# Kernel tuning notes

Hardware: AMD Instinct MI355X
Metric: run time of the kernel (lower is better)

The kernel has to match this reference:

```python
import jax, jax.numpy as jnp
import numpy as np

T, B, D, H, L = 256, 32, 512, 512, 3  # seq_len, batch, input_size, hidden_size, num_layers


def setup_inputs() -> dict:
    key = jax.random.key(0)
    ks = jax.random.split(key, 18)
    s = 0.02  # small init to keep gates out of saturation
    rn = lambda k, shape: (jax.random.normal(k, shape, dtype=jnp.float32) * s)
    return {
        "x": jax.random.normal(ks[0], (T, B, D), dtype=jnp.float32),
        "h0": jax.random.normal(ks[1], (L, B, H), dtype=jnp.float32),
        "c0": jax.random.normal(ks[2], (L, B, H), dtype=jnp.float32),
        # per-layer gate projections (torch Linear -> W in [in, out] layout)
        "W_i2h": rn(ks[3], (L, D, 3 * H)), "b_i2h": rn(ks[4], (L, 3 * H)),
        "W_h2h": rn(ks[5], (L, H, 3 * H)), "b_h2h": rn(ks[6], (L, 3 * H)),
        "W_wc": rn(ks[7], (L, D, H)),      "b_wc": rn(ks[8], (L, H)),
        # L x L gated-feedback weights: wg(input), ug(concat of all hiddens), uc(per-layer hidden)
        "W_wg": rn(ks[9], (L, L, D, H)),       "b_wg": rn(ks[10], (L, L, H)),
        "W_ug": rn(ks[11], (L, L, L * H, H)),  "b_ug": rn(ks[12], (L, L, H)),
        "W_uc": rn(ks[13], (L, L, H, H)),      "b_uc": rn(ks[14], (L, L, H)),
    }


def reference(x, h0, c0, W_i2h, b_i2h, W_h2h, b_h2h, W_wc, b_wc,
              W_wg, b_wg, W_ug, b_ug, W_uc, b_uc):
    num_layers, Hh = h0.shape[0], h0.shape[2]

    def step(carry, x_t):
        h, c = carry  # [L, B, H] each
        # concat of all previous hidden states along features: [B, L*H]
        nowH = jnp.transpose(h, (1, 0, 2)).reshape(h.shape[1], -1)
        inp = x_t
        hs, cs = [], []
        for l in range(num_layers):
            gates = jax.nn.sigmoid(inp @ W_i2h[l] + b_i2h[l]
                                   + h[l] @ W_h2h[l] + b_h2h[l])  # [B, 3H]
            i_g, f_g, o_g = jnp.split(gates, 3, axis=1)
            # global gates over all source layers _l: [L, B, H]
            gg = jax.nn.sigmoid(
                jnp.einsum('bd,ldh->lbh', inp, W_wg[l]) + b_wg[l][:, None, :]
                + jnp.einsum('bk,lkh->lbh', nowH, W_ug[l]) + b_ug[l][:, None, :])
            # gated contributions from each layer's previous hidden state
            uc = jnp.einsum('lbh,lhk->lbk', h, W_uc[l]) + b_uc[l][:, None, :]
            cand = jnp.tanh(inp @ W_wc[l] + b_wc[l] + jnp.sum(gg * uc, axis=0))
            c_new = f_g * c[l] + i_g * cand
            h_new = o_g * jnp.tanh(c_new)
            hs.append(h_new)
            cs.append(c_new)
            inp = h_new  # dropout == 0 -> identity
        return (jnp.stack(hs), jnp.stack(cs)), hs[-1]

    (h_n, c_n), out = jax.lax.scan(step, (h0, c0), x)
    return out, (h_n, c_n)
```

## Files before the change

kernel.cpp:

```cpp
#include <hip/hip_runtime.h>
#include <math.h>

#define TT 256
#define BB 32
#define DD 512
#define HH 512
#define H3 1536

static constexpr size_t SZ_I2HT = 3ull * H3 * HH;
static constexpr size_t SZ_H2HT = 3ull * H3 * HH;
static constexpr size_t SZ_WCT  = 3ull * HH * HH;
static constexpr size_t SZ_WGT  = 9ull * HH * HH;
static constexpr size_t SZ_UGT  = 9ull * HH * H3;
static constexpr size_t SZ_UCT  = 9ull * HH * HH;
static constexpr size_t SZ_ST   = 3ull * BB * HH;
static constexpr size_t SZ_GH   = 3ull * BB * H3;
static constexpr size_t SZ_UGP  = 3ull * 9 * BB * HH;
static constexpr size_t SZ_UCB  = 9ull * BB * HH;

static constexpr size_t OFF_I2HT = 0;
static constexpr size_t OFF_H2HT = OFF_I2HT + SZ_I2HT;
static constexpr size_t OFF_WCT  = OFF_H2HT + SZ_H2HT;
static constexpr size_t OFF_WGT  = OFF_WCT + SZ_WCT;
static constexpr size_t OFF_UGT  = OFF_WGT + SZ_WGT;
static constexpr size_t OFF_UCT  = OFF_UGT + SZ_UGT;
static constexpr size_t OFF_HST  = OFF_UCT + SZ_UCT;
static constexpr size_t OFF_CST  = OFF_HST + SZ_ST;
static constexpr size_t OFF_GH   = OFF_CST + SZ_ST;
static constexpr size_t OFF_UGP  = OFF_GH + SZ_GH;
static constexpr size_t OFF_UCB  = OFF_UGP + SZ_UGP;
static constexpr size_t WS_FLOATS = OFF_UCB + SZ_UCB;

struct KArgs {
  const float* x;
  const float *b_i2h, *b_h2h, *b_wg, *b_ug, *b_uc, *b_wc;
  const float *i2hT, *h2hT, *wcT, *wgT, *ugT, *ucT;
  float *hst, *cst, *gh, *ugp, *ucb, *out;
};

__device__ __forceinline__ float cload(const float* p) {
  return __hip_atomic_load(p, __ATOMIC_RELAXED, __HIP_MEMORY_SCOPE_AGENT);
}
__device__ __forceinline__ void cstore(float* p, float v) {
  __hip_atomic_store(p, v, __ATOMIC_RELAXED, __HIP_MEMORY_SCOPE_AGENT);
}
__device__ __forceinline__ float2 cload2(const float* p) {
  unsigned long long u = __hip_atomic_load(
      reinterpret_cast<const unsigned long long*>(p),
      __ATOMIC_RELAXED, __HIP_MEMORY_SCOPE_AGENT);
  return __builtin_bit_cast(float2, u);
}
__device__ __forceinline__ void cstore2(float* p, float2 v) {
  __hip_atomic_store(reinterpret_cast<unsigned long long*>(p),
                     __builtin_bit_cast(unsigned long long, v),
                     __ATOMIC_RELAXED, __HIP_MEMORY_SCOPE_AGENT);
}

__device__ unsigned int g_cnt[64 * 64];

__global__ void k_zero() {
  for (int i = threadIdx.x; i < 64 * 64; i += blockDim.x) g_cnt[i] = 0u;
}

__device__ __forceinline__ void poll_until(unsigned int target) {
  if (threadIdx.x < 64) {
    for (;;) {
      unsigned int s = __hip_atomic_load(&g_cnt[threadIdx.x * 64],
                                         __ATOMIC_RELAXED, __HIP_MEMORY_SCOPE_AGENT);
      s += __shfl_xor(s, 1);
      s += __shfl_xor(s, 2);
      s += __shfl_xor(s, 4);
      s += __shfl_xor(s, 8);
      s += __shfl_xor(s, 16);
      s += __shfl_xor(s, 32);
      if (s >= target) break;
      __builtin_amdgcn_s_sleep(8);
    }
  }
}

__device__ __forceinline__ void gbar_arrive(unsigned int target) {
  __syncthreads();
  if (threadIdx.x == 0) {
    __hip_atomic_fetch_add(&g_cnt[(blockIdx.x & 63) * 64], 1u,
                           __ATOMIC_RELAXED, __HIP_MEMORY_SCOPE_AGENT);
  }
  poll_until(target);
  __syncthreads();
}

__device__ __forceinline__ void gbar_wait(unsigned int target) {
  __syncthreads();
  poll_until(target);
  __syncthreads();
}

__global__ __launch_bounds__(256) void k_transpose(const float* __restrict__ in,
                                                   float* __restrict__ out,
                                                   int K, int N) {
  __shared__ float t[32][33];
  size_t mo = (size_t)blockIdx.z * K * N;
  in += mo; out += mo;
  int n0 = blockIdx.x * 32, k0 = blockIdx.y * 32;
  int c = threadIdx.x & 31, r0 = (threadIdx.x >> 5) * 4;
#pragma unroll
  for (int i = 0; i < 4; ++i) t[r0 + i][c] = in[(size_t)(k0 + r0 + i) * N + n0 + c];
  __syncthreads();
#pragma unroll
  for (int i = 0; i < 4; ++i) out[(size_t)(n0 + r0 + i) * K + k0 + c] = t[c][r0 + i];
}

__global__ void k_copy(const float* __restrict__ a, float* __restrict__ o, int n) {
  int i = blockIdx.x * blockDim.x + threadIdx.x;
  if (i < n) o[i] = a[i];
}

__device__ __forceinline__ int xslot(int g) { return g ^ ((g >> 4) & 7); }

__device__ __forceinline__ void stage_swz(const float* __restrict__ src,
                                          float* __restrict__ sx, int tid) {
#pragma unroll 8
  for (int fi = tid; fi < (BB * HH) / 4; fi += 256) {
    int b = fi >> 7, g = fi & 127;
    float4 v = reinterpret_cast<const float4*>(src)[fi];
    *reinterpret_cast<float4*>(&sx[b * HH + (xslot(g) << 2)]) = v;
  }
}

__device__ __forceinline__ void stage_swz_coh(const float* __restrict__ src,
                                              float* __restrict__ sx, int tid) {
#pragma unroll
  for (int half = 0; half < 2; ++half) {
    float4 v[8];
#pragma unroll
    for (int i = 0; i < 8; ++i) {
      int fi = tid + (half * 8 + i) * 256;
      const float* p = src + (size_t)fi * 4;
      asm volatile("global_load_dwordx4 %0, %1, off sc1" : "=v"(v[i]) : "v"(p));
    }
    asm volatile("s_waitcnt vmcnt(0)" ::: "memory");
#pragma unroll
    for (int i = 0; i < 8; ++i) {
      int fi = tid + (half * 8 + i) * 256;
      int b = fi >> 7, g = fi & 127;
      *reinterpret_cast<float4*>(&sx[b * HH + (xslot(g) << 2)]) = v[i];
    }
  }
}

__device__ __forceinline__ void stage_half_coh(const float* __restrict__ src,
                                               float* __restrict__ sx, int tid) {
  float4 v[8];
#pragma unroll
  for (int i = 0; i < 8; ++i) {
    int fi = tid + i * 256;
    const float* p = src + (size_t)fi * 4;
    asm volatile("global_load_dwordx4 %0, %1, off sc1" : "=v"(v[i]) : "v"(p));
  }
  asm volatile("s_waitcnt vmcnt(0)" ::: "memory");
#pragma unroll
  for (int i = 0; i < 8; ++i) {
    int fi = tid + i * 256;
    int b = fi >> 7, g = fi & 127;
    *reinterpret_cast<float4*>(&sx[b * HH + (xslot(g) << 2)]) = v[i];
  }
}

__device__ __forceinline__ float dot4(float4 x, float4 w) {
  return x.x * w.x + x.y * w.y + x.z * w.z + x.w * w.w;
}

__device__ __forceinline__ float sigm(float x) { return 1.0f / (1.0f + expf(-x)); }

__device__ __forceinline__ void phaseA_work(const KArgs& A, float* sx, float* scr) {
  const int tid = threadIdx.x;
  const int bid = blockIdx.x;
  const int src = bid / 160;
  const int blk = bid - src * 160;
  const int p = blk & 1;
  stage_half_coh(A.hst + ((size_t)src * BB + p * 16) * HH, sx, tid);
  __syncthreads();
  const int wid = tid >> 6;
  if (wid == 3) return;
  const int lane = tid & 63;
  const int cq = lane & 7, kc = lane >> 3;
  const int u = (blk >> 1) * 6 + wid * 2 + p;

  const float* wb; size_t wstride; size_t koff = 0;
  float* op; int opstride;
  const float* bias1 = nullptr; const float* bias2 = nullptr;
  int col0;
  if (u < 96) {
    int w = u >> 1; col0 = w * 32;
    wb = A.h2hT + (size_t)src * H3 * HH; wstride = HH;
    op = A.gh + (size_t)src * BB * H3; opstride = H3;
    bias1 = A.b_i2h + src * H3; bias2 = A.b_h2h + src * H3;
  } else if (u < 384) {
    int v = u - 96; int w = v >> 1;
    int q = w >> 4; col0 = (w & 15) * 32;
    wb = A.ugT + (size_t)q * HH * H3; wstride = H3; koff = (size_t)src * HH;
    op = A.ugp + (size_t)(src * 9 + q) * BB * HH; opstride = HH;
    if (src == 0) { bias1 = A.b_wg + q * HH; bias2 = A.b_ug + q * HH; }
  } else {
    int v = u - 384; int w = v >> 1;
    int qi = w >> 4; int q = qi * 3 + src; col0 = (w & 15) * 32;
    wb = A.ucT + (size_t)q * HH * HH; wstride = HH;
    op = A.ucb + (size_t)q * BB * HH; opstride = HH;
    bias1 = A.b_uc + q * HH;
  }

  const int cbase = col0 + cq * 4;
  const float* w0 = wb + (size_t)(cbase + 0) * wstride + koff;
  const float* w1 = wb + (size_t)(cbase + 1) * wstride + koff;
  const float* w2 = wb + (size_t)(cbase + 2) * wstride + koff;
  const float* w3 = wb + (size_t)(cbase + 3) * wstride + koff;
  const float* xb = sx;

  float acc[4][16];
#pragma unroll
  for (int c = 0; c < 4; ++c)
#pragma unroll
    for (int b = 0; b < 16; ++b) acc[c][b] = 0.f;

  for (int jt = 0; jt < 16; ++jt) {
    const int g = jt * 8 + kc;
    const int k = g << 2;
    float4 wv0 = *reinterpret_cast<const float4*>(w0 + k);
    float4 wv1 = *reinterpret_cast<const float4*>(w1 + k);
    float4 wv2 = *reinterpret_cast<const float4*>(w2 + k);
    float4 wv3 = *reinterpret_cast<const float4*>(w3 + k);
    const int so = xslot(g) << 2;
#pragma unroll
    for (int b = 0; b < 16; ++b) {
      float4 xv = *reinterpret_cast<const float4*>(&xb[b * HH + so]);
      acc[0][b] += dot4(xv, wv0);
      acc[1][b] += dot4(xv, wv1);
      acc[2][b] += dot4(xv, wv2);
      acc[3][b] += dot4(xv, wv3);
    }
  }

#pragma unroll
  for (int c = 0; c < 4; ++c)
#pragma unroll
    for (int b = 0; b < 16; ++b) {
      float v = acc[c][b];
      v += __shfl_xor(v, 8);
      v += __shfl_xor(v, 16);
      v += __shfl_xor(v, 32);
      acc[c][b] = v;
    }

  float* wscr = scr + wid * 512;
  if (kc == 0) {
#pragma unroll
    for (int c = 0; c < 4; ++c) {
#pragma unroll
      for (int b = 0; b < 16; b += 4) {
        *reinterpret_cast<float4*>(&wscr[cq * 64 + c * 16 + b]) =
            make_float4(acc[c][b], acc[c][b + 1], acc[c][b + 2], acc[c][b + 3]);
      }
    }
  }
  {
    const int bl = lane & 15;
    const int cg = lane >> 4;
    const int b = p * 16 + bl;
    float* orow = op + (size_t)b * opstride + col0 + cg * 8;
#pragma unroll
    for (int i = 0; i < 8; i += 2) {
      int cl0 = cg * 8 + i, cl1 = cl0 + 1;
      float v0 = wscr[(cl0 >> 2) * 64 + (cl0 & 3) * 16 + bl];
      float v1 = wscr[(cl1 >> 2) * 64 + (cl1 & 3) * 16 + bl];
      int col = col0 + cl0;
      if (bias1) { v0 += bias1[col]; v1 += bias1[col + 1]; }
      if (bias2) { v0 += bias2[col]; v1 += bias2[col + 1]; }
      cstore2(orow + i, make_float2(v0, v1));
    }
  }
}

__device__ __forceinline__ void phaseB_work(const KArgs& A, float* sx, float* scr, int l, int t) {
  const int tid = threadIdx.x;
  const int bid = blockIdx.x;
  if (l == 0) stage_swz(A.x + (size_t)t * BB * DD, sx, tid);
  else        stage_swz_coh(A.hst + (size_t)(l - 1) * BB * HH, sx, tid);
  __syncthreads();
  const int jq = tid & 7;
  const int kcl = (tid >> 3) & 7;
  const int wid = tid >> 6;
  const int jg = (bid & 7) + ((bid >> 5) << 3);
  const int bq = (bid >> 3) & 3;
  const int j0 = jg * 8;
  const int j = j0 + jq;
  const float* w0 = A.i2hT + ((size_t)l * H3 + j) * HH;
  const float* w1 = A.i2hT + ((size_t)l * H3 + HH + j) * HH;
  const float* w2 = A.i2hT + ((size_t)l * H3 + 2 * HH + j) * HH;
  const float* w3 = A.wgT + ((size_t)(l * 3 + 0) * HH + j) * HH;
  const float* w4 = A.wgT + ((size_t)(l * 3 + 1) * HH + j) * HH;
  const float* w5 = A.wgT + ((size_t)(l * 3 + 2) * HH + j) * HH;
  const float* w6 = A.wcT + ((size_t)l * HH + j) * HH;
  const float* xb = sx + (size_t)(bq * 8) * HH;

  float acc[7][8];
#pragma unroll
  for (int m = 0; m < 7; ++m)
#pragma unroll
    for (int b = 0; b < 8; ++b) acc[m][b] = 0.f;

  for (int jt = 0; jt < 4; ++jt) {
    const int g = wid * 32 + jt * 8 + kcl;
    const int k = g << 2;
    float4 v0 = *reinterpret_cast<const float4*>(w0 + k);
    float4 v1 = *reinterpret_cast<const float4*>(w1 + k);
    float4 v2 = *reinterpret_cast<const float4*>(w2 + k);
    float4 v3 = *reinterpret_cast<const float4*>(w3 + k);
    float4 v4 = *reinterpret_cast<const float4*>(w4 + k);
    float4 v5 = *reinterpret_cast<const float4*>(w5 + k);
    float4 v6 = *reinterpret_cast<const float4*>(w6 + k);
    const int so = xslot(g) << 2;
#pragma unroll
    for (int b = 0; b < 8; ++b) {
      float4 xv = *reinterpret_cast<const float4*>(&xb[b * HH + so]);
      acc[0][b] += dot4(xv, v0);
      acc[1][b] += dot4(xv, v1);
      acc[2][b] += dot4(xv, v2);
      acc[3][b] += dot4(xv, v3);
      acc[4][b] += dot4(xv, v4);
      acc[5][b] += dot4(xv, v5);
      acc[6][b] += dot4(xv, v6);
    }
  }
#pragma unroll
  for (int m = 0; m < 7; ++m)
#pragma unroll
    for (int b = 0; b < 8; ++b) {
      float v = acc[m][b];
      v += __shfl_xor(v, 8);
      v += __shfl_xor(v, 16);
      v += __shfl_xor(v, 32);
      acc[m][b] = v;
    }
  if ((tid & 63) < 8) {
    float* pp = scr + wid * 448 + jq * 56;
#pragma unroll
    for (int m = 0; m < 7; ++m) {
      *reinterpret_cast<float4*>(&pp[m * 8 + 0]) =
          make_float4(acc[m][0], acc[m][1], acc[m][2], acc[m][3]);
      *reinterpret_cast<float4*>(&pp[m * 8 + 4]) =
          make_float4(acc[m][4], acc[m][5], acc[m][6], acc[m][7]);
    }
  }
  __syncthreads();
  if (tid < 64) {
    const int jr = tid & 7, br = tid >> 3;
    float a[7];
#pragma unroll
    for (int m = 0; m < 7; ++m) {
      const int o = jr * 56 + m * 8 + br;
      a[m] = scr[o] + scr[448 + o] + scr[896 + o] + scr[1344 + o];
    }
    const int jj = j0 + jr;
    const int b = bq * 8 + br;
    const size_t bh_ = (size_t)b * HH + jj;
    const float* gh_l = A.gh + (size_t)l * BB * H3;
    float si = sigm(a[0] + cload(&gh_l[(size_t)b * H3 + jj]));
    float sf = sigm(a[1] + cload(&gh_l[(size_t)b * H3 + HH + jj]));
    float so = sigm(a[2] + cload(&gh_l[(size_t)b * H3 + 2 * HH + jj]));
    const size_t CH = 9ull * BB * HH;
    size_t o0 = ((size_t)(l * 3 + 0) * BB + b) * HH + jj;
    size_t o1 = ((size_t)(l * 3 + 1) * BB + b) * HH + jj;
    size_t o2 = ((size_t)(l * 3 + 2) * BB + b) * HH + jj;
    float g0 = sigm(a[3] + cload(&A.ugp[o0]) + cload(&A.ugp[o0 + CH]) + cload(&A.ugp[o0 + 2 * CH]));
    float g1 = sigm(a[4] + cload(&A.ugp[o1]) + cload(&A.ugp[o1 + CH]) + cload(&A.ugp[o1 + 2 * CH]));
    float g2 = sigm(a[5] + cload(&A.ugp[o2]) + cload(&A.ugp[o2 + CH]) + cload(&A.ugp[o2 + 2 * CH]));
    float accc = a[6] + A.b_wc[l * HH + jj]
               + g0 * cload(&A.ucb[o0]) + g1 * cload(&A.ucb[o1]) + g2 * cload(&A.ucb[o2]);
    float cand = tanhf(accc);
    float* cp = A.cst + (size_t)l * BB * HH + bh_;
    float* hp = A.hst + (size_t)l * BB * HH + bh_;
    float cn = sf * cload(cp) + si * cand;
    float hn = so * tanhf(cn);
    cstore(cp, cn);
    cstore(hp, hn);
    if (l == 2) A.out[(size_t)t * BB * HH + bh_] = hn;
  }
}

__global__ __launch_bounds__(256, 2) void k_persist(KArgs A) {
  __shared__ float sx[BB * HH];
  __shared__ float scr[2048];
  unsigned int tgt = 0;
  const unsigned int nb = gridDim.x;
  for (int t = 0; t < TT; ++t) {
    phaseA_work(A, sx, scr);
    tgt += nb;
    gbar_arrive(tgt);
    for (int l = 0; l < 3; ++l) {
      tgt += 256;
      if (blockIdx.x < 256) {
        phaseB_work(A, sx, scr, l, t);
        gbar_arrive(tgt);
      } else if (l == 2) {
        gbar_wait(tgt);
      }
    }
  }
  float* dst = A.out + (size_t)TT * BB * HH;
  for (size_t i = (size_t)blockIdx.x * 256 + threadIdx.x; i < 2 * SZ_ST;
       i += (size_t)gridDim.x * 256) {
    if (i < SZ_ST) dst[i] = cload(A.hst + i);
    else dst[i] = cload(A.cst + (i - SZ_ST));
  }
}

__global__ __launch_bounds__(256, 2) void k_phaseA(KArgs A) {
  __shared__ float sx[BB * HH];
  __shared__ float scr[2048];
  phaseA_work(A, sx, scr);
}
__global__ __launch_bounds__(256, 2) void k_phaseB(KArgs A, int l, int t) {
  __shared__ float sx[BB * HH];
  __shared__ float scr[2048];
  phaseB_work(A, sx, scr, l, t);
}

extern "C" void kernel_launch(void* const* d_in, const int* in_sizes, int n_in,
                              void* d_out, int out_size, void* d_ws, size_t ws_size,
                              hipStream_t stream) {
  const float* x     = (const float*)d_in[0];
  const float* h0    = (const float*)d_in[1];
  const float* c0    = (const float*)d_in[2];
  const float* W_i2h = (const float*)d_in[3];
  const float* b_i2h = (const float*)d_in[4];
  const float* W_h2h = (const float*)d_in[5];
  const float* b_h2h = (const float*)d_in[6];
  const float* W_wc  = (const float*)d_in[7];
  const float* b_wc  = (const float*)d_in[8];
  const float* W_wg  = (const float*)d_in[9];
  const float* b_wg  = (const float*)d_in[10];
  const float* W_ug  = (const float*)d_in[11];
  const float* b_ug  = (const float*)d_in[12];
  const float* W_uc  = (const float*)d_in[13];
  const float* b_uc  = (const float*)d_in[14];
  float* out = (float*)d_out;
  float* ws  = (float*)d_ws;

  if (ws_size < WS_FLOATS * sizeof(float)) return;

  float* i2hT = ws + OFF_I2HT;
  float* h2hT = ws + OFF_H2HT;
  float* wcT  = ws + OFF_WCT;
  float* wgT  = ws + OFF_WGT;
  float* ugT  = ws + OFF_UGT;
  float* ucT  = ws + OFF_UCT;
  float* hst  = ws + OFF_HST;
  float* cst  = ws + OFF_CST;
  float* gh   = ws + OFF_GH;
  float* ugp  = ws + OFF_UGP;
  float* ucb  = ws + OFF_UCB;

  dim3 b256(256);
  hipLaunchKernelGGL(k_transpose, dim3(48, 16, 3), b256, 0, stream, W_i2h, i2hT, 512, 1536);
  hipLaunchKernelGGL(k_transpose, dim3(48, 16, 3), b256, 0, stream, W_h2h, h2hT, 512, 1536);
  hipLaunchKernelGGL(k_transpose, dim3(16, 16, 3), b256, 0, stream, W_wc, wcT, 512, 512);
  hipLaunchKernelGGL(k_transpose, dim3(16, 16, 9), b256, 0, stream, W_wg, wgT, 512, 512);
  hipLaunchKernelGGL(k_transpose, dim3(16, 48, 9), b256, 0, stream, W_ug, ugT, 1536, 512);
  hipLaunchKernelGGL(k_transpose, dim3(16, 16, 9), b256, 0, stream, W_uc, ucT, 512, 512);
  hipLaunchKernelGGL(k_copy, dim3(192), b256, 0, stream, h0, hst, (int)SZ_ST);
  hipLaunchKernelGGL(k_copy, dim3(192), b256, 0, stream, c0, cst, (int)SZ_ST);
  hipLaunchKernelGGL(k_zero, dim3(1), dim3(256), 0, stream);

  KArgs ka;
  ka.x = x;
  ka.b_i2h = b_i2h; ka.b_h2h = b_h2h; ka.b_wg = b_wg; ka.b_ug = b_ug;
  ka.b_uc = b_uc; ka.b_wc = b_wc;
  ka.i2hT = i2hT; ka.h2hT = h2hT; ka.wcT = wcT; ka.wgT = wgT;
  ka.ugT = ugT; ka.ucT = ucT;
  ka.hst = hst; ka.cst = cst; ka.gh = gh; ka.ugp = ugp; ka.ucb = ucb;
  ka.out = out;

  void* params[1] = {&ka};
  hipError_t ce = hipLaunchCooperativeKernel((const void*)k_persist, dim3(480), dim3(256),
                                             params, 0, stream);
  if (ce != hipSuccess) {
    for (int t = 0; t < TT; ++t) {
      hipLaunchKernelGGL(k_phaseA, dim3(480), b256, 0, stream, ka);
      for (int l = 0; l < 3; ++l)
        hipLaunchKernelGGL(k_phaseB, dim3(256), b256, 0, stream, ka, l, t);
    }
    hipLaunchKernelGGL(k_copy, dim3(192), b256, 0, stream, hst,
                       out + (size_t)TT * BB * HH, (int)SZ_ST);
    hipLaunchKernelGGL(k_copy, dim3(192), b256, 0, stream, cst,
                       out + (size_t)TT * BB * HH + SZ_ST, (int)SZ_ST);
  }
}
```

Measured before the change: 17.18 ms.

## Pipeline phase A of next timestep with phase B layers via double buffers

Splits the persistent cooperative grid into 256 blocks that run the sequential per-layer phase B and 224 blocks that compute the phase A hidden-state projections for the next timestep. Each source layer's projection starts as soon as that layer's new hidden state is ready, using separate counters and double-buffered ugp/ucb scratch. The aim is to hide phase A behind the layer chain and drop the full-grid barriers. It needs extra workspace, falls back to the old path if that is not available, and puts more load on fewer blocks.

```diff
diff --git a/kernel.cpp b/kernel.cpp
--- a/kernel.cpp
+++ b/kernel.cpp
@@ -30,12 +30,15 @@
 static constexpr size_t OFF_UGP  = OFF_GH + SZ_GH;
 static constexpr size_t OFF_UCB  = OFF_UGP + SZ_UGP;
 static constexpr size_t WS_FLOATS = OFF_UCB + SZ_UCB;
+static constexpr size_t OFF_UGP2 = OFF_UCB + SZ_UCB;
+static constexpr size_t OFF_UCB2 = OFF_UGP2 + SZ_UGP;
+static constexpr size_t WS_FLOATS2 = OFF_UCB2 + SZ_UCB;
 
 struct KArgs {
   const float* x;
   const float *b_i2h, *b_h2h, *b_wg, *b_ug, *b_uc, *b_wc;
   const float *i2hT, *h2hT, *wcT, *wgT, *ugT, *ucT;
-  float *hst, *cst, *gh, *ugp, *ucb, *out;
+  float *hst, *cst, *gh, *ugp, *ucb, *ugp2, *ucb2, *out;
 };
 
 __device__ __forceinline__ float cload(const float* p) {
@@ -43,12 +46,6 @@
 }
 __device__ __forceinline__ void cstore(float* p, float v) {
   __hip_atomic_store(p, v, __ATOMIC_RELAXED, __HIP_MEMORY_SCOPE_AGENT);
-}
-__device__ __forceinline__ float2 cload2(const float* p) {
-  unsigned long long u = __hip_atomic_load(
-      reinterpret_cast<const unsigned long long*>(p),
-      __ATOMIC_RELAXED, __HIP_MEMORY_SCOPE_AGENT);
-  return __builtin_bit_cast(float2, u);
 }
 __device__ __forceinline__ void cstore2(float* p, float2 v) {
   __hip_atomic_store(reinterpret_cast<unsigned long long*>(p),
@@ -56,16 +53,28 @@
                      __ATOMIC_RELAXED, __HIP_MEMORY_SCOPE_AGENT);
 }
 
-__device__ unsigned int g_cnt[64 * 64];
+__device__ unsigned int g_cntA[64 * 64];
+__device__ unsigned int g_cntB[64 * 64];
 
 __global__ void k_zero() {
-  for (int i = threadIdx.x; i < 64 * 64; i += blockDim.x) g_cnt[i] = 0u;
-}
-
-__device__ __forceinline__ void poll_until(unsigned int target) {
+  for (int i = threadIdx.x; i < 64 * 64; i += blockDim.x) {
+    g_cntA[i] = 0u;
+    g_cntB[i] = 0u;
+  }
+}
+
+__device__ __forceinline__ void arrive(unsigned int* cnt) {
+  __syncthreads();
+  if (threadIdx.x == 0) {
+    __hip_atomic_fetch_add(&cnt[(blockIdx.x & 63) * 64], 1u,
+                           __ATOMIC_RELAXED, __HIP_MEMORY_SCOPE_AGENT);
+  }
+}
+
+__device__ __forceinline__ void wait_for(unsigned int* cnt, unsigned int target) {
   if (threadIdx.x < 64) {
     for (;;) {
-      unsigned int s = __hip_atomic_load(&g_cnt[threadIdx.x * 64],
+      unsigned int s = __hip_atomic_load(&cnt[threadIdx.x * 64],
                                          __ATOMIC_RELAXED, __HIP_MEMORY_SCOPE_AGENT);
       s += __shfl_xor(s, 1);
       s += __shfl_xor(s, 2);
@@ -77,21 +86,6 @@
       __builtin_amdgcn_s_sleep(8);
     }
   }
-}
-
-__device__ __forceinline__ void gbar_arrive(unsigned int target) {
-  __syncthreads();
-  if (threadIdx.x == 0) {
-    __hip_atomic_fetch_add(&g_cnt[(blockIdx.x & 63) * 64], 1u,
-                           __ATOMIC_RELAXED, __HIP_MEMORY_SCOPE_AGENT);
-  }
-  poll_until(target);
-  __syncthreads();
-}
-
-__device__ __forceinline__ void gbar_wait(unsigned int target) {
-  __syncthreads();
-  poll_until(target);
   __syncthreads();
 }
 
@@ -172,7 +166,107 @@
 
 __device__ __forceinline__ float sigm(float x) { return 1.0f / (1.0f + expf(-x)); }
 
-__device__ __forceinline__ void phaseA_work(const KArgs& A, float* sx, float* scr) {
+__device__ __forceinline__ void phaseA_unit(const KArgs& A, const float* sx,
+                                            float* scr, int wid, int lane,
+                                            int src, int u,
+                                            float* ugp_buf, float* ucb_buf) {
+  const int cq = lane & 7, kc = lane >> 3;
+  const float* wb; size_t wstride; size_t koff = 0;
+  float* op; int opstride;
+  const float* bias1 = nullptr; const float* bias2 = nullptr;
+  int col0, bh;
+  if (u < 96) {
+    int w = u >> 1; bh = u & 1; col0 = w * 32;
+    wb = A.h2hT + (size_t)src * H3 * HH; wstride = HH;
+    op = A.gh + (size_t)src * BB * H3; opstride = H3;
+    bias1 = A.b_i2h + src * H3; bias2 = A.b_h2h + src * H3;
+  } else if (u < 384) {
+    int v = u - 96; int w = v >> 1; bh = v & 1;
+    int q = w >> 4; col0 = (w & 15) * 32;
+    wb = A.ugT + (size_t)q * HH * H3; wstride = H3; koff = (size_t)src * HH;
+    op = ugp_buf + (size_t)(src * 9 + q) * BB * HH; opstride = HH;
+    if (src == 0) { bias1 = A.b_wg + q * HH; bias2 = A.b_ug + q * HH; }
+  } else {
+    int v = u - 384; int w = v >> 1; bh = v & 1;
+    int qi = w >> 4; int q = qi * 3 + src; col0 = (w & 15) * 32;
+    wb = A.ucT + (size_t)q * HH * HH; wstride = HH;
+    op = ucb_buf + (size_t)q * BB * HH; opstride = HH;
+    bias1 = A.b_uc + q * HH;
+  }
+
+  const int cbase = col0 + cq * 4;
+  const float* w0 = wb + (size_t)(cbase + 0) * wstride + koff;
+  const float* w1 = wb + (size_t)(cbase + 1) * wstride + koff;
+  const float* w2 = wb + (size_t)(cbase + 2) * wstride + koff;
+  const float* w3 = wb + (size_t)(cbase + 3) * wstride + koff;
+  const float* xb = sx + (size_t)(bh * 16) * HH;
+
+  float acc[4][16];
+#pragma unroll
+  for (int c = 0; c < 4; ++c)
+#pragma unroll
+    for (int b = 0; b < 16; ++b) acc[c][b] = 0.f;
+
+  for (int jt = 0; jt < 16; ++jt) {
+    const int g = jt * 8 + kc;
+    const int k = g << 2;
+    float4 wv0 = *reinterpret_cast<const float4*>(w0 + k);
+    float4 wv1 = *reinterpret_cast<const float4*>(w1 + k);
+    float4 wv2 = *reinterpret_cast<const float4*>(w2 + k);
+    float4 wv3 = *reinterpret_cast<const float4*>(w3 + k);
+    const int so = xslot(g) << 2;
+#pragma unroll
+    for (int b = 0; b < 16; ++b) {
+      float4 xv = *reinterpret_cast<const float4*>(&xb[b * HH + so]);
+      acc[0][b] += dot4(xv, wv0);
+      acc[1][b] += dot4(xv, wv1);
+      acc[2][b] += dot4(xv, wv2);
+      acc[3][b] += dot4(xv, wv3);
+    }
+  }
+
+#pragma unroll
+  for (int c = 0; c < 4; ++c)
+#pragma unroll
+    for (int b = 0; b < 16; ++b) {
+      float v = acc[c][b];
+      v += __shfl_xor(v, 8);
+      v += __shfl_xor(v, 16);
+      v += __shfl_xor(v, 32);
+      acc[c][b] = v;
+    }
+
+  float* wscr = scr + wid * 512;
+  if (kc == 0) {
+#pragma unroll
+    for (int c = 0; c < 4; ++c) {
+#pragma unroll
+      for (int b = 0; b < 16; b += 4) {
+        *reinterpret_cast<float4*>(&wscr[cq * 64 + c * 16 + b]) =
+            make_float4(acc[c][b], acc[c][b + 1], acc[c][b + 2], acc[c][b + 3]);
+      }
+    }
+  }
+  {
+    const int bl = lane & 15;
+    const int cg = lane >> 4;
+    const int b = bh * 16 + bl;
+    float* orow = op + (size_t)b * opstride + col0 + cg * 8;
+#pragma unroll
+    for (int i = 0; i < 8; i += 2) {
+      int cl0 = cg * 8 + i, cl1 = cl0 + 1;
+      float v0 = wscr[(cl0 >> 2) * 64 + (cl0 & 3) * 16 + bl];
+      float v1 = wscr[(cl1 >> 2) * 64 + (cl1 & 3) * 16 + bl];
+      int col = col0 + cl0;
+      if (bias1) { v0 += bias1[col]; v1 += bias1[col + 1]; }
+      if (bias2) { v0 += bias2[col]; v1 += bias2[col + 1]; }
+      cstore2(orow + i, make_float2(v0, v1));
+    }
+  }
+}
+
+__device__ __forceinline__ void phaseA_work(const KArgs& A, float* sx, float* scr,
+                                            float* ugp_buf, float* ucb_buf) {
   const int tid = threadIdx.x;
   const int bid = blockIdx.x;
   const int src = bid / 160;
@@ -183,104 +277,13 @@
   const int wid = tid >> 6;
   if (wid == 3) return;
   const int lane = tid & 63;
-  const int cq = lane & 7, kc = lane >> 3;
   const int u = (blk >> 1) * 6 + wid * 2 + p;
-
-  const float* wb; size_t wstride; size_t koff = 0;
-  float* op; int opstride;
-  const float* bias1 = nullptr; const float* bias2 = nullptr;
-  int col0;
-  if (u < 96) {
-    int w = u >> 1; col0 = w * 32;
-    wb = A.h2hT + (size_t)src * H3 * HH; wstride = HH;
-    op = A.gh + (size_t)src * BB * H3; opstride = H3;
-    bias1 = A.b_i2h + src * H3; bias2 = A.b_h2h + src * H3;
-  } else if (u < 384) {
-    int v = u - 96; int w = v >> 1;
-    int q = w >> 4; col0 = (w & 15) * 32;
-    wb = A.ugT + (size_t)q * HH * H3; wstride = H3; koff = (size_t)src * HH;
-    op = A.ugp + (size_t)(src * 9 + q) * BB * HH; opstride = HH;
-    if (src == 0) { bias1 = A.b_wg + q * HH; bias2 = A.b_ug + q * HH; }
-  } else {
-    int v = u - 384; int w = v >> 1;
-    int qi = w >> 4; int q = qi * 3 + src; col0 = (w & 15) * 32;
-    wb = A.ucT + (size_t)q * HH * HH; wstride = HH;
-    op = A.ucb + (size_t)q * BB * HH; opstride = HH;
-    bias1 = A.b_uc + q * HH;
-  }
-
-  const int cbase = col0 + cq * 4;
-  const float* w0 = wb + (size_t)(cbase + 0) * wstride + koff;
-  const float* w1 = wb + (size_t)(cbase + 1) * wstride + koff;
-  const float* w2 = wb + (size_t)(cbase + 2) * wstride + koff;
-  const float* w3 = wb + (size_t)(cbase + 3) * wstride + koff;
-  const float* xb = sx;
-
-  float acc[4][16];
-#pragma unroll
-  for (int c = 0; c < 4; ++c)
-#pragma unroll
-    for (int b = 0; b < 16; ++b) acc[c][b] = 0.f;
-
-  for (int jt = 0; jt < 16; ++jt) {
-    const int g = jt * 8 + kc;
-    const int k = g << 2;
-    float4 wv0 = *reinterpret_cast<const float4*>(w0 + k);
-    float4 wv1 = *reinterpret_cast<const float4*>(w1 + k);
-    float4 wv2 = *reinterpret_cast<const float4*>(w2 + k);
-    float4 wv3 = *reinterpret_cast<const float4*>(w3 + k);
-    const int so = xslot(g) << 2;
-#pragma unroll
-    for (int b = 0; b < 16; ++b) {
-      float4 xv = *reinterpret_cast<const float4*>(&xb[b * HH + so]);
-      acc[0][b] += dot4(xv, wv0);
-      acc[1][b] += dot4(xv, wv1);
-      acc[2][b] += dot4(xv, wv2);
-      acc[3][b] += dot4(xv, wv3);
-    }
-  }
-
-#pragma unroll
-  for (int c = 0; c < 4; ++c)
-#pragma unroll
-    for (int b = 0; b < 16; ++b) {
-      float v = acc[c][b];
-      v += __shfl_xor(v, 8);
-      v += __shfl_xor(v, 16);
-      v += __shfl_xor(v, 32);
-      acc[c][b] = v;
-    }
-
-  float* wscr = scr + wid * 512;
-  if (kc == 0) {
-#pragma unroll
-    for (int c = 0; c < 4; ++c) {
-#pragma unroll
-      for (int b = 0; b < 16; b += 4) {
-        *reinterpret_cast<float4*>(&wscr[cq * 64 + c * 16 + b]) =
-            make_float4(acc[c][b], acc[c][b + 1], acc[c][b + 2], acc[c][b + 3]);
-      }
-    }
-  }
-  {
-    const int bl = lane & 15;
-    const int cg = lane >> 4;
-    const int b = p * 16 + bl;
-    float* orow = op + (size_t)b * opstride + col0 + cg * 8;
-#pragma unroll
-    for (int i = 0; i < 8; i += 2) {
-      int cl0 = cg * 8 + i, cl1 = cl0 + 1;
-      float v0 = wscr[(cl0 >> 2) * 64 + (cl0 & 3) * 16 + bl];
-      float v1 = wscr[(cl1 >> 2) * 64 + (cl1 & 3) * 16 + bl];
-      int col = col0 + cl0;
-      if (bias1) { v0 += bias1[col]; v1 += bias1[col + 1]; }
-      if (bias2) { v0 += bias2[col]; v1 += bias2[col + 1]; }
-      cstore2(orow + i, make_float2(v0, v1));
-    }
-  }
-}
-
-__device__ __forceinline__ void phaseB_work(const KArgs& A, float* sx, float* scr, int l, int t) {
+  phaseA_unit(A, sx - (size_t)(p * 16) * HH, scr, wid, lane, src, u, ugp_buf, ucb_buf);
+}
+
+__device__ __forceinline__ void phaseB_work(const KArgs& A, float* sx, float* scr,
+                                            int l, int t,
+                                            const float* ugp_t, const float* ucb_t) {
   const int tid = threadIdx.x;
   const int bid = blockIdx.x;
   if (l == 0) stage_swz(A.x + (size_t)t * BB * DD, sx, tid);
@@ -371,11 +374,11 @@
     size_t o0 = ((size_t)(l * 3 + 0) * BB + b) * HH + jj;
     size_t o1 = ((size_t)(l * 3 + 1) * BB + b) * HH + jj;
     size_t o2 = ((size_t)(l * 3 + 2) * BB + b) * HH + jj;
-    float g0 = sigm(a[3] + cload(&A.ugp[o0]) + cload(&A.ugp[o0 + CH]) + cload(&A.ugp[o0 + 2 * CH]));
-    float g1 = sigm(a[4] + cload(&A.ugp[o1]) + cload(&A.ugp[o1 + CH]) + cload(&A.ugp[o1 + 2 * CH]));
-    float g2 = sigm(a[5] + cload(&A.ugp[o2]) + cload(&A.ugp[o2 + CH]) + cload(&A.ugp[o2 + 2 * CH]));
+    float g0 = sigm(a[3] + cload(&ugp_t[o0]) + cload(&ugp_t[o0 + CH]) + cload(&ugp_t[o0 + 2 * CH]));
+    float g1 = sigm(a[4] + cload(&ugp_t[o1]) + cload(&ugp_t[o1 + CH]) + cload(&ugp_t[o1 + 2 * CH]));
+    float g2 = sigm(a[5] + cload(&ugp_t[o2]) + cload(&ugp_t[o2 + CH]) + cload(&ugp_t[o2 + 2 * CH]));
     float accc = a[6] + A.b_wc[l * HH + jj]
-               + g0 * cload(&A.ucb[o0]) + g1 * cload(&A.ucb[o1]) + g2 * cload(&A.ucb[o2]);
+               + g0 * cload(&ucb_t[o0]) + g1 * cload(&ucb_t[o1]) + g2 * cload(&ucb_t[o2]);
     float cand = tanhf(accc);
     float* cp = A.cst + (size_t)l * BB * HH + bh_;
     float* hp = A.hst + (size_t)l * BB * HH + bh_;
@@ -387,22 +390,86 @@
   }
 }
 
-__global__ __launch_bounds__(256, 2) void k_persist(KArgs A) {
+__global__ __launch_bounds__(256, 2) void k_persist_pipe(KArgs A) {
+  __shared__ float sx[BB * HH];
+  __shared__ float scr[2048];
+  const int bid = blockIdx.x;
+  const int tid = threadIdx.x;
+  if (bid < 256) {
+    for (int t = 0; t < TT; ++t) {
+      wait_for(g_cntA, (unsigned)(t + 1) * 224u);
+      float* ugp_t = (t & 1) ? A.ugp2 : A.ugp;
+      float* ucb_t = (t & 1) ? A.ucb2 : A.ucb;
+      const unsigned base = 3u * (unsigned)t * 256u;
+      phaseB_work(A, sx, scr, 0, t, ugp_t, ucb_t);
+      arrive(g_cntB);
+      wait_for(g_cntB, base + 256u);
+      phaseB_work(A, sx, scr, 1, t, ugp_t, ucb_t);
+      arrive(g_cntB);
+      wait_for(g_cntB, base + 512u);
+      phaseB_work(A, sx, scr, 2, t, ugp_t, ucb_t);
+      arrive(g_cntB);
+    }
+    wait_for(g_cntB, 3u * TT * 256u);
+  } else {
+    const int a = bid - 256;
+    const int src = (a < 75) ? 0 : (a < 150) ? 1 : 2;
+    const int i0 = a - ((src == 0) ? 0 : (src == 1) ? 75 : 150);
+    const int nblk = (src < 2) ? 75 : 74;
+    const int lo = (i0 * 480) / nblk;
+    const int hi = ((i0 + 1) * 480) / nblk;
+    const int wid = tid >> 6, lane = tid & 63;
+    stage_swz_coh(A.hst + (size_t)src * BB * HH, sx, tid);
+    __syncthreads();
+    for (int it = 0; lo + it * 4 < hi; ++it) {
+      int u = lo + it * 4 + wid;
+      if (u < hi) phaseA_unit(A, sx, scr, wid, lane, src, u, A.ugp, A.ucb);
+    }
+    arrive(g_cntA);
+    for (int t = 0; t < TT; ++t) {
+      if (t + 1 < TT) {
+        wait_for(g_cntB, 3u * (unsigned)t * 256u + (unsigned)(src + 1) * 256u);
+        float* ugp_n = ((t + 1) & 1) ? A.ugp2 : A.ugp;
+        float* ucb_n = ((t + 1) & 1) ? A.ucb2 : A.ucb;
+        stage_swz_coh(A.hst + (size_t)src * BB * HH, sx, tid);
+        __syncthreads();
+        for (int it = 0; lo + it * 4 < hi; ++it) {
+          int u = lo + it * 4 + wid;
+          if (u < hi) phaseA_unit(A, sx, scr, wid, lane, src, u, ugp_n, ucb_n);
+        }
+        arrive(g_cntA);
+      } else {
+        wait_for(g_cntB, 3u * TT * 256u);
+      }
+    }
+  }
+  float* dst = A.out + (size_t)TT * BB * HH;
+  for (size_t i = (size_t)blockIdx.x * 256 + threadIdx.x; i < 2 * SZ_ST;
+       i += (size_t)gridDim.x * 256) {
+    if (i < SZ_ST) dst[i] = cload(A.hst + i);
+    else dst[i] = cload(A.cst + (i - SZ_ST));
+  }
+}
+
+__global__ __launch_bounds__(256, 2) void k_persist_np(KArgs A) {
   __shared__ float sx[BB * HH];
   __shared__ float scr[2048];
   unsigned int tgt = 0;
   const unsigned int nb = gridDim.x;
   for (int t = 0; t < TT; ++t) {
-    phaseA_work(A, sx, scr);
+    phaseA_work(A, sx, scr, A.ugp, A.ucb);
     tgt += nb;
-    gbar_arrive(tgt);
+    arrive(g_cntB);
+    wait_for(g_cntB, tgt);
     for (int l = 0; l < 3; ++l) {
       tgt += 256;
       if (blockIdx.x < 256) {
-        phaseB_work(A, sx, scr, l, t);
-        gbar_arrive(tgt);
+        phaseB_work(A, sx, scr, l, t, A.ugp, A.ucb);
+        arrive(g_cntB);
+        wait_for(g_cntB, tgt);
       } else if (l == 2) {
-        gbar_wait(tgt);
+        __syncthreads();
+        wait_for(g_cntB, tgt);
       }
     }
   }
@@ -417,12 +484,12 @@
 __global__ __launch_bounds__(256, 2) void k_phaseA(KArgs A) {
   __shared__ float sx[BB * HH];
   __shared__ float scr[2048];
-  phaseA_work(A, sx, scr);
+  phaseA_work(A, sx, scr, A.ugp, A.ucb);
 }
 __global__ __launch_bounds__(256, 2) void k_phaseB(KArgs A, int l, int t) {
   __shared__ float sx[BB * HH];
   __shared__ float scr[2048];
-  phaseB_work(A, sx, scr, l, t);
+  phaseB_work(A, sx, scr, l, t, A.ugp, A.ucb);
 }
 
 extern "C" void kernel_launch(void* const* d_in, const int* in_sizes, int n_in,
@@ -447,6 +514,7 @@
   float* ws  = (float*)d_ws;
 
   if (ws_size < WS_FLOATS * sizeof(float)) return;
+  const bool pipe = ws_size >= WS_FLOATS2 * sizeof(float);
 
   float* i2hT = ws + OFF_I2HT;
   float* h2hT = ws + OFF_H2HT;
@@ -478,11 +546,14 @@
   ka.i2hT = i2hT; ka.h2hT = h2hT; ka.wcT = wcT; ka.wgT = wgT;
   ka.ugT = ugT; ka.ucT = ucT;
   ka.hst = hst; ka.cst = cst; ka.gh = gh; ka.ugp = ugp; ka.ucb = ucb;
+  ka.ugp2 = pipe ? (ws + OFF_UGP2) : ugp;
+  ka.ucb2 = pipe ? (ws + OFF_UCB2) : ucb;
   ka.out = out;
 
   void* params[1] = {&ka};
-  hipError_t ce = hipLaunchCooperativeKernel((const void*)k_persist, dim3(480), dim3(256),
-                                             params, 0, stream);
+  hipError_t ce = hipLaunchCooperativeKernel(
+      pipe ? (const void*)k_persist_pipe : (const void*)k_persist_np,
+      dim3(480), dim3(256), params, 0, stream);
   if (ce != hipSuccess) {
     for (int t = 0; t < TT; ++t) {
       hipLaunchKernelGGL(k_phaseA, dim3(480), b256, 0, stream, ka);
```

After: 30.46 ms. 77.2% more time.
